# Kernel tuning notes

Hardware: AMD Instinct MI355X
Metric: run time of the kernel (lower is better)

## Reference

```python
import jax, jax.numpy as jnp
import numpy as np

B, T, E, H = 2, 1024, 2048, 32
D = E // H
GROUP = (0.25, 0.25, 0.25, 0.25)
NEG = float(np.finfo(np.float32).min)


def quant_per_token(t, n_bits):
    # smoothquant-style: clamp(absmax, 1e-5) / qmax, per last-dim row
    qmax = 2 ** (n_bits - 1) - 1
    s = jnp.clip(jnp.abs(t).max(-1, keepdims=True), 1e-5, None) / qmax
    return jnp.round(t / s) * s


def w8a8_linear(x, W, b, quant_out=False):
    xq = quant_per_token(x, 8)           # per-token act quant
    Wq = quant_per_token(W, 8)           # per-output-channel weight quant (W: [out, in])
    y = xq @ Wq.T + b
    return quant_per_token(y, 8) if quant_out else y


def to_heads(x):
    # [B, T, E] -> [B*H, T, D]
    return x.reshape(B, T, H, D).transpose(0, 2, 1, 3).reshape(B * H, T, D)


def setup_inputs() -> dict:
    key = jax.random.key(0)
    ks = jax.random.split(key, 9)
    hidden_states = jax.random.normal(ks[0], (B, T, E), jnp.float32)
    causal = jnp.where(jnp.tril(jnp.ones((T, T), bool)), 0.0, NEG).astype(jnp.float32)
    attention_mask = jnp.broadcast_to(causal[None, None], (B, 1, T, T))
    w = 0.02
    return {
        'hidden_states': hidden_states,
        'attention_mask': attention_mask,
        'Wq': jax.random.normal(ks[1], (E, E), jnp.float32) * w,
        'bq': jax.random.normal(ks[2], (E,), jnp.float32) * w,
        'Wk': jax.random.normal(ks[3], (E, E), jnp.float32) * w,
        'bk': jax.random.normal(ks[4], (E,), jnp.float32) * w,
        'Wv': jax.random.normal(ks[5], (E, E), jnp.float32) * w,
        'bv': jax.random.normal(ks[6], (E,), jnp.float32) * w,
        'Wo': jax.random.normal(ks[7], (E, E), jnp.float32) * w,
        'bo': jax.random.normal(ks[8], (E,), jnp.float32) * w,
    }


def reference(hidden_states, attention_mask, Wq, bq, Wk, bk, Wv, bv, Wo, bo):
    scaling = D ** -0.5
    q = w8a8_linear(hidden_states, Wq, bq, quant_out=True) * scaling  # [B,T,E]
    k = w8a8_linear(hidden_states, Wk, bk)                            # [B,T,E]
    v = w8a8_linear(hidden_states, Wv, bv)                            # [B,T,E]

    # ---- heavy-hitter scoring pass (pre-4bit-quant K) ----
    q1, k1 = to_heads(q), to_heads(k)                                 # [BH,T,D]
    aw = jnp.einsum('btd,bsd->bts', q1, k1)                           # [BH,T,T]
    aw = aw.reshape(B, H, T, T) + attention_mask
    aw = jnp.maximum(aw, NEG).reshape(B * H, T, T)
    tmp_attn = jax.nn.softmax(aw, axis=-1)
    acc = tmp_attn.sum(axis=1).sum(axis=0)[None, :]                   # [1,T]
    row_vector = jnp.arange(T, 0, -1).astype(jnp.float32)[None, :]    # T, T-1, ..., 1
    acc = acc / row_vector / (B * H)

    # ---- group-wise top-k heavy-hitter selection ----
    range_size_or = int(T / len(GROUP) / 2)
    start = 1
    idx_list = []
    for i, ratio in enumerate(GROUP):
        rs = int(T * ratio)
        end = min(start + rs - 1, T) if i < len(GROUP) - 1 else T
        partial = acc[:, start - 1:end]
        _, ti = jax.lax.top_k(partial, range_size_or)
        idx_list.append(ti + start - 1)
        start = end + 1
    topk_idx = jnp.concatenate(idx_list, axis=-1).reshape(-1)

    # ---- mixed-precision K quantization ----
    k_abs = jnp.abs(k)
    # fake_quant_mix (8-bit): amax(...)[0] in torch indexes batch 0 -> scales [T,1]
    s_mix = jnp.clip(k_abs.max(-1, keepdims=True)[0] / 127.0, 1e-5, None)  # [T,1]
    k_imp = jnp.round(k / s_mix) * s_mix
    # fake_quant (4-bit, per-row): clamp then divide by 7
    s4 = jnp.clip(k_abs.max(-1, keepdims=True), 1e-5, None) / 7.0
    kq = jnp.round(k / s4) * s4
    kq = kq.at[:, topk_idx, :].set(k_imp[:, topk_idx, :])
    # fake_quant_v (4-bit, per-tensor)
    sv = jnp.clip(jnp.abs(v).max(), 1e-5, None) / 7.0
    vq = jnp.round(v / sv) * sv

    # ---- actual attention with quantized K/V ----
    q2, k2, v2 = to_heads(q), to_heads(kq), to_heads(vq)
    aw2 = jnp.einsum('btd,bsd->bts', q2, k2).reshape(B, H, T, T) + attention_mask
    aw2 = jnp.maximum(aw2, NEG).reshape(B * H, T, T)
    probs = jax.nn.softmax(aw2, axis=-1)
    out = jnp.einsum('bts,bsd->btd', probs, v2)                       # [BH,T,D]
    out = out.reshape(B, H, T, D).transpose(0, 2, 1, 3).reshape(B, T, E)
    return w8a8_linear(out, Wo, bo)
```

## Files before the change

### kernel.cpp

```cpp
#include <hip/hip_runtime.h>
#include <stdint.h>

#define NEG_INF (-__builtin_inff())
#define L2E 1.4426950408889634f

namespace {
constexpr int kT   = 1024;
constexpr int kE   = 2048;
}

using bf16x8 = __attribute__((ext_vector_type(8))) short;
using f32x4  = __attribute__((ext_vector_type(4))) float;
using i32x4  = __attribute__((ext_vector_type(4))) int;

#define MFMA_BF16(a, b, c) __builtin_amdgcn_mfma_f32_16x16x32_bf16((a), (b), (c), 0, 0, 0)
#define MFMA_I8(a, b, c)   __builtin_amdgcn_mfma_i32_16x16x64_i8((a), (b), (c), 0, 0, 0)

__device__ __forceinline__ void gload16(const void* g, void* l) {
  __builtin_amdgcn_global_load_lds((const __attribute__((address_space(1))) unsigned*)g,
                                   (__attribute__((address_space(3))) unsigned*)l, 16, 0, 0);
}
__device__ __forceinline__ unsigned bfr(float x) {
  unsigned u = __float_as_uint(x);
  return (u + 0x7FFFu + ((u >> 16) & 1u)) >> 16;
}
__device__ __forceinline__ float bf2f(unsigned h) { return __uint_as_float(h << 16); }
__device__ __forceinline__ unsigned pk2(float a, float b) { return bfr(a) | (bfr(b) << 16); }
__device__ __forceinline__ float fexp2(float x) { return __builtin_amdgcn_exp2f(x); }

__device__ __forceinline__ float waveReduceMax(float v) {
#pragma unroll
  for (int o = 32; o > 0; o >>= 1) v = fmaxf(v, __shfl_down(v, o, 64));
  return v;
}
__device__ __forceinline__ float waveReduceSum(float v) {
#pragma unroll
  for (int o = 32; o > 0; o >>= 1) v += __shfl_down(v, o, 64);
  return v;
}
__device__ __forceinline__ float blockMax256(float v, float* r4) {
  const int tid = threadIdx.x;
  float wm = waveReduceMax(v);
  if ((tid & 63) == 0) r4[tid >> 6] = wm;
  __syncthreads();
  float bm = fmaxf(fmaxf(r4[0], r4[1]), fmaxf(r4[2], r4[3]));
  __syncthreads();
  return bm;
}

__global__ __launch_bounds__(256) void k_rowquant_all(const float* __restrict__ Xh,
                                                      const float* __restrict__ W0,
                                                      const float* __restrict__ W1,
                                                      const float* __restrict__ W2,
                                                      const float* __restrict__ W3,
                                                      int8_t* __restrict__ Qh,
                                                      int8_t* __restrict__ Q0,
                                                      int8_t* __restrict__ Q1,
                                                      int8_t* __restrict__ Q2,
                                                      int8_t* __restrict__ Q3,
                                                      float* __restrict__ sX,
                                                      float* __restrict__ sWall,
                                                      unsigned* __restrict__ vmax) {
  const int y = blockIdx.y;
  const float* X = (y == 0) ? Xh : (y == 1) ? W0 : (y == 2) ? W1 : (y == 3) ? W2 : W3;
  int8_t* Qp = (y == 0) ? Qh : (y == 1) ? Q0 : (y == 2) ? Q1 : (y == 3) ? Q2 : Q3;
  const int row = blockIdx.x;
  const int tid = threadIdx.x;
  if (row == 0 && y == 0 && tid == 0) *vmax = 0u;
  const float* x = X + (size_t)row * kE;
  __shared__ float r4[4];
  float am = 0.f;
  float4 v[2];
#pragma unroll
  for (int it = 0; it < 2; ++it) {
    v[it] = *reinterpret_cast<const float4*>(x + (size_t)(it * 256 + tid) * 4);
    am = fmaxf(am, fmaxf(fmaxf(fabsf(v[it].x), fabsf(v[it].y)), fmaxf(fabsf(v[it].z), fabsf(v[it].w))));
  }
  const float bm = blockMax256(am, r4);
  const float s = fmaxf(bm, 1e-5f) / 127.f;
  int8_t* xq = Qp + (size_t)row * kE;
#pragma unroll
  for (int it = 0; it < 2; ++it) {
    const int i = (it * 256 + tid) * 4;
    char4 q;
    q.x = (char)(int)rintf(v[it].x / s);
    q.y = (char)(int)rintf(v[it].y / s);
    q.z = (char)(int)rintf(v[it].z / s);
    q.w = (char)(int)rintf(v[it].w / s);
    *reinterpret_cast<char4*>(xq + i) = q;
  }
  if (tid == 0) {
    if (y == 0) sX[row] = s;
    else sWall[(y - 1) * kE + row] = s;
  }
}

__global__ __launch_bounds__(256) void k_rowquant_i8(const float* __restrict__ X,
                                                     int8_t* __restrict__ Xq,
                                                     float* __restrict__ S) {
  const int row = blockIdx.x;
  const int tid = threadIdx.x;
  const float* x = X + (size_t)row * kE;
  __shared__ float r4[4];
  float am = 0.f;
  float4 v[2];
#pragma unroll
  for (int it = 0; it < 2; ++it) {
    v[it] = *reinterpret_cast<const float4*>(x + (size_t)(it * 256 + tid) * 4);
    am = fmaxf(am, fmaxf(fmaxf(fabsf(v[it].x), fabsf(v[it].y)), fmaxf(fabsf(v[it].z), fabsf(v[it].w))));
  }
  const float bm = blockMax256(am, r4);
  const float s = fmaxf(bm, 1e-5f) / 127.f;
  int8_t* xq = Xq + (size_t)row * kE;
#pragma unroll
  for (int it = 0; it < 2; ++it) {
    const int i = (it * 256 + tid) * 4;
    char4 q;
    q.x = (char)(int)rintf(v[it].x / s);
    q.y = (char)(int)rintf(v[it].y / s);
    q.z = (char)(int)rintf(v[it].z / s);
    q.w = (char)(int)rintf(v[it].w / s);
    *reinterpret_cast<char4*>(xq + i) = q;
  }
  if (tid == 0) S[row] = s;
}

__global__ __launch_bounds__(256) void k_prep(const float* __restrict__ Qb,
                                              const float* __restrict__ Kb,
                                              const float* __restrict__ Vb,
                                              short* __restrict__ qi,
                                              float* __restrict__ sqg,
                                              short* __restrict__ khi,
                                              short* __restrict__ klo,
                                              float* __restrict__ s4,
                                              float* __restrict__ smix,
                                              unsigned* __restrict__ vmax) {
  const int row = blockIdx.x;
  const int tid = threadIdx.x;
  __shared__ float r4[4];

  {
    const float* x = Qb + (size_t)row * kE;
    float am = 0.f;
    float4 v[2];
#pragma unroll
    for (int it = 0; it < 2; ++it) {
      v[it] = *reinterpret_cast<const float4*>(x + (size_t)(it * 256 + tid) * 4);
      am = fmaxf(am, fmaxf(fmaxf(fabsf(v[it].x), fabsf(v[it].y)), fmaxf(fabsf(v[it].z), fabsf(v[it].w))));
    }
    const float bm = blockMax256(am, r4);
    const float s = fmaxf(bm, 1e-5f) / 127.f;
#pragma unroll
    for (int it = 0; it < 2; ++it) {
      const int i = (it * 256 + tid) * 4;
      short4 q;
      q.x = (short)bfr(rintf(v[it].x / s));
      q.y = (short)bfr(rintf(v[it].y / s));
      q.z = (short)bfr(rintf(v[it].z / s));
      q.w = (short)bfr(rintf(v[it].w / s));
      *reinterpret_cast<short4*>(qi + (size_t)row * kE + i) = q;
    }
    if (tid == 0) sqg[row] = s * 0.125f;
  }

  {
    const float* x = Kb + (size_t)row * kE;
    float am = 0.f;
    float4 v[2];
#pragma unroll
    for (int it = 0; it < 2; ++it) {
      v[it] = *reinterpret_cast<const float4*>(x + (size_t)(it * 256 + tid) * 4);
      am = fmaxf(am, fmaxf(fmaxf(fabsf(v[it].x), fabsf(v[it].y)), fmaxf(fabsf(v[it].z), fabsf(v[it].w))));
    }
    const float bm = blockMax256(am, r4);
#pragma unroll
    for (int it = 0; it < 2; ++it) {
      const int i = (it * 256 + tid) * 4;
      short4 hh, ll;
      unsigned hb;
      hb = bfr(v[it].x); hh.x = (short)hb; ll.x = (short)bfr(v[it].x - bf2f(hb));
      hb = bfr(v[it].y); hh.y = (short)hb; ll.y = (short)bfr(v[it].y - bf2f(hb));
      hb = bfr(v[it].z); hh.z = (short)hb; ll.z = (short)bfr(v[it].z - bf2f(hb));
      hb = bfr(v[it].w); hh.w = (short)hb; ll.w = (short)bfr(v[it].w - bf2f(hb));
      *reinterpret_cast<short4*>(khi + (size_t)row * kE + i) = hh;
      *reinterpret_cast<short4*>(klo + (size_t)row * kE + i) = ll;
    }
    if (tid == 0) {
      s4[row] = fmaxf(bm, 1e-5f) / 7.f;
      if (row < kT) smix[row] = fmaxf(bm / 127.f, 1e-5f);
    }
  }

  {
    const float* x = Vb + (size_t)row * kE;
    float am = 0.f;
#pragma unroll
    for (int it = 0; it < 2; ++it) {
      const float4 v = *reinterpret_cast<const float4*>(x + (size_t)(it * 256 + tid) * 4);
      am = fmaxf(am, fmaxf(fmaxf(fabsf(v.x), fabsf(v.y)), fmaxf(fabsf(v.z), fabsf(v.w))));
    }
    const float bm = blockMax256(am, r4);
    if (tid == 0) atomicMax(vmax, __float_as_uint(bm));
  }
}

__global__ __launch_bounds__(256) void k_kint(const float* __restrict__ Kb,
                                              const float* __restrict__ s4,
                                              const float* __restrict__ smix,
                                              const int* __restrict__ sel,
                                              short* __restrict__ ki,
                                              float* __restrict__ skg) {
  const int row = blockIdx.x;
  const int tid = threadIdx.x;
  const int t = row & (kT - 1);
  const float s = sel[t] ? smix[t] : s4[row];
  const float* x = Kb + (size_t)row * kE;
#pragma unroll
  for (int it = 0; it < 2; ++it) {
    const int i = (it * 256 + tid) * 4;
    const float4 v = *reinterpret_cast<const float4*>(x + i);
    short4 q;
    q.x = (short)bfr(rintf(v.x / s));
    q.y = (short)bfr(rintf(v.y / s));
    q.z = (short)bfr(rintf(v.z / s));
    q.w = (short)bfr(rintf(v.w / s));
    *reinterpret_cast<short4*>(ki + (size_t)row * kE + i) = q;
  }
  if (tid == 0) skg[row] = s;
}

__global__ __launch_bounds__(256) void k_vint(const float* __restrict__ Vb,
                                              const unsigned* __restrict__ vmax,
                                              short* __restrict__ vt) {
  const int tt = blockIdx.x;
  const int bh = blockIdx.y;
  const int b = bh >> 5, h = bh & 31;
  const float sv = fmaxf(__uint_as_float(*vmax), 1e-5f) / 7.f;
  __shared__ short tr[64][80];
  const int tid = threadIdx.x;
#pragma unroll
  for (int i = 0; i < 4; ++i) {
    const int e = i * 256 + tid;
    const int tok = e >> 4, d4 = (e & 15) * 4;
    const float4 v = *reinterpret_cast<const float4*>(
        &Vb[(size_t)(b * kT + tt * 64 + tok) * kE + h * 64 + d4]);
    tr[d4 + 0][tok] = (short)bfr(rintf(v.x / sv));
    tr[d4 + 1][tok] = (short)bfr(rintf(v.y / sv));
    tr[d4 + 2][tok] = (short)bfr(rintf(v.z / sv));
    tr[d4 + 3][tok] = (short)bfr(rintf(v.w / sv));
  }
  __syncthreads();
#pragma unroll
  for (int i = 0; i < 2; ++i) {
    const int e = i * 256 + tid;
    const int d = e >> 3, u = e & 7;
    const bf16x8 row = *reinterpret_cast<const bf16x8*>(&tr[d][u * 8]);
    *reinterpret_cast<bf16x8*>(&vt[(size_t)(bh * 64 + d) * kT + tt * 64 + u * 8]) = row;
  }
}

__device__ __forceinline__ void gemm_i8_body(int m0, int n0,
                                             const int8_t* __restrict__ A,
                                             const float* __restrict__ sa,
                                             const int8_t* __restrict__ Bw,
                                             const float* __restrict__ sw,
                                             const float* __restrict__ bias,
                                             float* __restrict__ Y,
                                             int8_t* As0, int8_t* As1,
                                             int8_t* Bs0, int8_t* Bs1) {
  int8_t* Asb[2] = {As0, As1};
  int8_t* Bsb[2] = {Bs0, Bs1};
  const int tid = threadIdx.x;
  const int lane = tid & 63, w = tid >> 6;
  const int g = lane >> 4, c16 = lane & 15;
  const int wm = (w >> 1) * 64, wn = (w & 1) * 64;
  const int rsw = (c16 >> 1) & 3;

  const i32x4 zero = {0, 0, 0, 0};
  i32x4 acc[4][4];
#pragma unroll
  for (int i = 0; i < 4; ++i)
#pragma unroll
    for (int j = 0; j < 4; ++j) acc[i][j] = zero;

  const int srow = tid >> 2, su = tid & 3;
  const int ssw = (srow >> 1) & 3;
  auto stage = [&](int buf, int k0) {
#pragma unroll
    for (int i = 0; i < 2; ++i) {
      const int row = i * 64 + srow;
      const int uoff = ((su ^ ssw) << 4);
      gload16(A + (size_t)(m0 + row) * kE + k0 + uoff, &Asb[buf][row * 64 + su * 16]);
      gload16(Bw + (size_t)(n0 + row) * kE + k0 + uoff, &Bsb[buf][row * 64 + su * 16]);
    }
  };

  stage(0, 0);
  __syncthreads();
  int cur = 0;
  for (int k0 = 0; k0 < kE; k0 += 64) {
    if (k0 + 64 < kE) stage(cur ^ 1, k0 + 64);
    i32x4 av[4], bv[4];
#pragma unroll
    for (int f = 0; f < 4; ++f) {
      const int ar = wm + f * 16 + c16;
      av[f] = *reinterpret_cast<const i32x4*>(&Asb[cur][ar * 64 + ((g ^ rsw) << 4)]);
      const int br = wn + f * 16 + c16;
      bv[f] = *reinterpret_cast<const i32x4*>(&Bsb[cur][br * 64 + ((g ^ rsw) << 4)]);
    }
#pragma unroll
    for (int fm = 0; fm < 4; ++fm)
#pragma unroll
      for (int fn = 0; fn < 4; ++fn) acc[fm][fn] = MFMA_I8(av[fm], bv[fn], acc[fm][fn]);
    __syncthreads();
    cur ^= 1;
  }

#pragma unroll
  for (int fn = 0; fn < 4; ++fn) {
    const int n = n0 + wn + fn * 16 + c16;
    const float swn = sw[n], bn = bias[n];
#pragma unroll
    for (int fm = 0; fm < 4; ++fm) {
#pragma unroll
      for (int r = 0; r < 4; ++r) {
        const int m = m0 + wm + fm * 16 + g * 4 + r;
        Y[(size_t)m * kE + n] = (float)acc[fm][fn][r] * sa[m] * swn + bn;
      }
    }
  }
}

__global__ __launch_bounds__(256) void k_gemm_i8(const int8_t* __restrict__ A,
                                                 const float* __restrict__ sa,
                                                 const int8_t* __restrict__ Bw,
                                                 const float* __restrict__ sw,
                                                 const float* __restrict__ bias,
                                                 float* __restrict__ Y) {
  __shared__ int8_t As[2][128 * 64];
  __shared__ int8_t Bs[2][128 * 64];
  const int linear = blockIdx.x + (blockIdx.y << 4);
  const int nid = (linear & 7) * 32 + (linear >> 3);
  const int x = nid & 15, y = nid >> 4;
  gemm_i8_body(y * 128, x * 128, A, sa, Bw, sw, bias, Y, As[0], As[1], Bs[0], Bs[1]);
}

__global__ __launch_bounds__(256) void k_gemm_qkv(const int8_t* __restrict__ A,
                                                  const float* __restrict__ sa,
                                                  const int8_t* __restrict__ Wq,
                                                  const int8_t* __restrict__ Wk,
                                                  const int8_t* __restrict__ Wv,
                                                  const float* __restrict__ sWall,
                                                  const float* __restrict__ bq,
                                                  const float* __restrict__ bk,
                                                  const float* __restrict__ bv,
                                                  float* __restrict__ qb,
                                                  float* __restrict__ kb,
                                                  float* __restrict__ vb) {
  __shared__ int8_t As[2][128 * 64];
  __shared__ int8_t Bs[2][128 * 64];
  const int linear = blockIdx.x + (blockIdx.y << 4) + (blockIdx.z << 8);
  const int nid = (linear & 7) * 96 + (linear >> 3);
  const int x = nid & 15, y = (nid >> 4) & 15, z = nid >> 8;
  const int8_t* Bw = (z == 0) ? Wq : (z == 1) ? Wk : Wv;
  const float* sw = sWall + (size_t)z * kE;
  const float* bias = (z == 0) ? bq : (z == 1) ? bk : bv;
  float* Y = (z == 0) ? qb : (z == 1) ? kb : vb;
  gemm_i8_body(y * 128, x * 128, A, sa, Bw, sw, bias, Y, As[0], As[1], Bs[0], Bs[1]);
}

__global__ __launch_bounds__(256) void k_attn1(const short* __restrict__ qi,
                                               const short* __restrict__ khi,
                                               const short* __restrict__ klo,
                                               const float* __restrict__ sqg,
                                               float* __restrict__ accPart) {
  const int r1 = blockIdx.x, r2 = 15 - r1, bh = blockIdx.y;
  const int b = bh >> 5, h = bh & 31;
  const int tid = threadIdx.x, lane = tid & 63, w = tid >> 6;
  const int g = lane >> 4, c16 = lane & 15;
  const int swz = c16 & 7;

  __shared__ short qs1[64 * 64];
  __shared__ short qs2[64 * 64];
  __shared__ short hbuf[2][64 * 64];
  __shared__ short lbuf[2][64 * 64];
  __shared__ float accL[1024];
  __shared__ float Arow[128], Crow[128];

  for (int i = tid; i < 1024; i += 256) accL[i] = 0.f;

  const int st8 = tid >> 3, su = tid & 7;
  {
    const int tokb1 = b * kT + r1 * 64;
    const int tokb2 = b * kT + r2 * 64;
#pragma unroll
    for (int i = 0; i < 2; ++i) {
      const int tok = i * 32 + st8;
      const int co = ((su ^ (tok & 7)) << 3);
      gload16(qi + (size_t)(tokb1 + tok) * kE + h * 64 + co, &qs1[tok * 64 + su * 8]);
      gload16(qi + (size_t)(tokb2 + tok) * kE + h * 64 + co, &qs2[tok * 64 + su * 8]);
    }
  }
  auto stage = [&](int buf, int kt) {
    const int tokb = b * kT + kt * 64;
#pragma unroll
    for (int i = 0; i < 2; ++i) {
      const int tok = i * 32 + st8;
      const size_t gsrc = (size_t)(tokb + tok) * kE + h * 64 + ((su ^ (tok & 7)) << 3);
      gload16(khi + gsrc, &hbuf[buf][tok * 64 + su * 8]);
      gload16(klo + gsrc, &lbuf[buf][tok * 64 + su * 8]);
    }
  };

  stage(0, 0);
  __syncthreads();

  const int qrow = w * 16 + c16;
  const bf16x8 q1_0 = *reinterpret_cast<const bf16x8*>(&qs1[qrow * 64 + ((g ^ swz) << 3)]);
  const bf16x8 q1_1 = *reinterpret_cast<const bf16x8*>(&qs1[qrow * 64 + (((4 + g) ^ swz) << 3)]);
  const bf16x8 q2_0 = *reinterpret_cast<const bf16x8*>(&qs2[qrow * 64 + ((g ^ swz) << 3)]);
  const bf16x8 q2_1 = *reinterpret_cast<const bf16x8*>(&qs2[qrow * 64 + (((4 + g) ^ swz) << 3)]);
  const float A1c = sqg[b * kT + r1 * 64 + qrow] * L2E;
  const float A2c = sqg[b * kT + r2 * 64 + qrow] * L2E;

  float m1 = NEG_INF, l1 = 0.f, m2_ = NEG_INF, l2 = 0.f;
  int cur = 0;

  for (int kt = 0; kt <= r2; ++kt) {
    if (kt < r2) stage(cur ^ 1, kt + 1);
    const bool act1 = kt <= r1;
    float p1[4][4], p2[4][4];
    float pm1 = NEG_INF, pm2 = NEG_INF;
#pragma unroll
    for (int f = 0; f < 4; ++f) {
      const int tokl = f * 16 + c16;
      const bf16x8 ah0 = *reinterpret_cast<const bf16x8*>(&hbuf[cur][tokl * 64 + ((g ^ swz) << 3)]);
      const bf16x8 ah1 = *reinterpret_cast<const bf16x8*>(&hbuf[cur][tokl * 64 + (((4 + g) ^ swz) << 3)]);
      const bf16x8 al0 = *reinterpret_cast<const bf16x8*>(&lbuf[cur][tokl * 64 + ((g ^ swz) << 3)]);
      const bf16x8 al1 = *reinterpret_cast<const bf16x8*>(&lbuf[cur][tokl * 64 + (((4 + g) ^ swz) << 3)]);
      f32x4 sB = {0.f, 0.f, 0.f, 0.f};
      sB = MFMA_BF16(ah0, q2_0, sB);
      sB = MFMA_BF16(ah1, q2_1, sB);
      sB = MFMA_BF16(al0, q2_0, sB);
      sB = MFMA_BF16(al1, q2_1, sB);
      f32x4 sA = {0.f, 0.f, 0.f, 0.f};
      if (act1) {
        sA = MFMA_BF16(ah0, q1_0, sA);
        sA = MFMA_BF16(ah1, q1_1, sA);
        sA = MFMA_BF16(al0, q1_0, sA);
        sA = MFMA_BF16(al1, q1_1, sA);
      }
#pragma unroll
      for (int r = 0; r < 4; ++r) {
        const int tokd = f * 16 + g * 4 + r;
        float s2 = sB[r] * A2c;
        if (kt == r2 && tokd > qrow) s2 = NEG_INF;
        p2[f][r] = s2;
        pm2 = fmaxf(pm2, s2);
        float s1 = sA[r] * A1c;
        if (kt == r1 && tokd > qrow) s1 = NEG_INF;
        p1[f][r] = s1;
        pm1 = fmaxf(pm1, s1);
      }
    }
    {
      pm2 = fmaxf(pm2, __shfl_xor(pm2, 16));
      pm2 = fmaxf(pm2, __shfl_xor(pm2, 32));
      const bool upd = pm2 > m2_ + 8.f;
      const float mn = upd ? fmaxf(m2_, pm2) : m2_;
      const float fsc = fexp2(m2_ - mn);
      float rs = 0.f;
#pragma unroll
      for (int f = 0; f < 4; ++f)
#pragma unroll
        for (int r = 0; r < 4; ++r) rs += fexp2(p2[f][r] - mn);
      rs += __shfl_xor(rs, 16);
      rs += __shfl_xor(rs, 32);
      l2 = l2 * fsc + rs;
      m2_ = mn;
    }
    if (act1) {
      pm1 = fmaxf(pm1, __shfl_xor(pm1, 16));
      pm1 = fmaxf(pm1, __shfl_xor(pm1, 32));
      const bool upd = pm1 > m1 + 8.f;
      const float mn = upd ? fmaxf(m1, pm1) : m1;
      const float fsc = fexp2(m1 - mn);
      float rs = 0.f;
#pragma unroll
      for (int f = 0; f < 4; ++f)
#pragma unroll
        for (int r = 0; r < 4; ++r) rs += fexp2(p1[f][r] - mn);
      rs += __shfl_xor(rs, 16);
      rs += __shfl_xor(rs, 32);
      l1 = l1 * fsc + rs;
      m1 = mn;
    }
    __syncthreads();
    cur ^= 1;
  }

  if (g == 0) {
    Arow[qrow] = A1c;
    Crow[qrow] = -(m1 + __builtin_amdgcn_logf(l1));
    Arow[64 + qrow] = A2c;
    Crow[64 + qrow] = -(m2_ + __builtin_amdgcn_logf(l2));
  }
  stage(0, 0);
  __syncthreads();

  bf16x8 qa1_0[4], qa1_1[4], qa2_0[4], qa2_1[4];
  float Ar1[4][4], Cr1[4][4], Ar2[4][4], Cr2[4][4];
#pragma unroll
  for (int f = 0; f < 4; ++f) {
    const int qr = f * 16 + c16;
    qa1_0[f] = *reinterpret_cast<const bf16x8*>(&qs1[qr * 64 + ((g ^ swz) << 3)]);
    qa1_1[f] = *reinterpret_cast<const bf16x8*>(&qs1[qr * 64 + (((4 + g) ^ swz) << 3)]);
    qa2_0[f] = *reinterpret_cast<const bf16x8*>(&qs2[qr * 64 + ((g ^ swz) << 3)]);
    qa2_1[f] = *reinterpret_cast<const bf16x8*>(&qs2[qr * 64 + (((4 + g) ^ swz) << 3)]);
#pragma unroll
    for (int r = 0; r < 4; ++r) {
      const int tokd = f * 16 + g * 4 + r;
      Ar1[f][r] = Arow[tokd];
      Cr1[f][r] = Crow[tokd];
      Ar2[f][r] = Arow[64 + tokd];
      Cr2[f][r] = Crow[64 + tokd];
    }
  }

  const int ktokL = w * 16 + c16;
  cur = 0;
  for (int kt = 0; kt <= r2; ++kt) {
    if (kt < r2) stage(cur ^ 1, kt + 1);
    const bf16x8 kh0 = *reinterpret_cast<const bf16x8*>(&hbuf[cur][ktokL * 64 + ((g ^ swz) << 3)]);
    const bf16x8 kh1 = *reinterpret_cast<const bf16x8*>(&hbuf[cur][ktokL * 64 + (((4 + g) ^ swz) << 3)]);
    const bf16x8 kl0 = *reinterpret_cast<const bf16x8*>(&lbuf[cur][ktokL * 64 + ((g ^ swz) << 3)]);
    const bf16x8 kl1 = *reinterpret_cast<const bf16x8*>(&lbuf[cur][ktokL * 64 + (((4 + g) ^ swz) << 3)]);
    float csum = 0.f;
    if (kt < r2) {
#pragma unroll
      for (int f = 0; f < 4; ++f) {
        f32x4 sf = {0.f, 0.f, 0.f, 0.f};
        sf = MFMA_BF16(qa2_0[f], kh0, sf);
        sf = MFMA_BF16(qa2_1[f], kh1, sf);
        sf = MFMA_BF16(qa2_0[f], kl0, sf);
        sf = MFMA_BF16(qa2_1[f], kl1, sf);
#pragma unroll
        for (int r = 0; r < 4; ++r) csum += fexp2(fmaf(sf[r], Ar2[f][r], Cr2[f][r]));
      }
    } else {
#pragma unroll
      for (int f = 0; f < 4; ++f) {
        f32x4 sf = {0.f, 0.f, 0.f, 0.f};
        sf = MFMA_BF16(qa2_0[f], kh0, sf);
        sf = MFMA_BF16(qa2_1[f], kh1, sf);
        sf = MFMA_BF16(qa2_0[f], kl0, sf);
        sf = MFMA_BF16(qa2_1[f], kl1, sf);
#pragma unroll
        for (int r = 0; r < 4; ++r) {
          const float v = fexp2(fmaf(sf[r], Ar2[f][r], Cr2[f][r]));
          if (ktokL <= (f * 16 + g * 4 + r)) csum += v;
        }
      }
    }
    if (kt <= r1) {
      if (kt < r1) {
#pragma unroll
        for (int f = 0; f < 4; ++f) {
          f32x4 sf = {0.f, 0.f, 0.f, 0.f};
          sf = MFMA_BF16(qa1_0[f], kh0, sf);
          sf = MFMA_BF16(qa1_1[f], kh1, sf);
          sf = MFMA_BF16(qa1_0[f], kl0, sf);
          sf = MFMA_BF16(qa1_1[f], kl1, sf);
#pragma unroll
          for (int r = 0; r < 4; ++r) csum += fexp2(fmaf(sf[r], Ar1[f][r], Cr1[f][r]));
        }
      } else {
#pragma unroll
        for (int f = 0; f < 4; ++f) {
          f32x4 sf = {0.f, 0.f, 0.f, 0.f};
          sf = MFMA_BF16(qa1_0[f], kh0, sf);
          sf = MFMA_BF16(qa1_1[f], kh1, sf);
          sf = MFMA_BF16(qa1_0[f], kl0, sf);
          sf = MFMA_BF16(qa1_1[f], kl1, sf);
#pragma unroll
          for (int r = 0; r < 4; ++r) {
            const float v = fexp2(fmaf(sf[r], Ar1[f][r], Cr1[f][r]));
            if (ktokL <= (f * 16 + g * 4 + r)) csum += v;
          }
        }
      }
    }
    csum += __shfl_xor(csum, 16);
    csum += __shfl_xor(csum, 32);
    if (g == 0) accL[kt * 64 + ktokL] += csum;
    __syncthreads();
    cur ^= 1;
  }

  for (int i = tid; i < 1024; i += 256)
    accPart[(size_t)(bh * 8 + r1) * 1024 + i] = accL[i];
}

__global__ __launch_bounds__(256) void k_accreduce(const float* __restrict__ part,
                                                   float* __restrict__ acc) {
  const int j = blockIdx.x;
  const int tid = threadIdx.x;
  float s = 0.f;
  for (int p = tid; p < 512; p += 256) s += part[(size_t)p * 1024 + j];
  __shared__ float r4[4];
  const float ws = waveReduceSum(s);
  if ((tid & 63) == 0) r4[tid >> 6] = ws;
  __syncthreads();
  if (tid == 0) {
    const float t = r4[0] + r4[1] + r4[2] + r4[3];
    acc[j] = t / (float)(kT - j) / 64.f;
  }
}

__global__ __launch_bounds__(256) void k_topk(const float* __restrict__ acc,
                                              int* __restrict__ sel) {
  const int gq = blockIdx.x;
  const int i = threadIdx.x;
  __shared__ float v[256];
  const float vi = acc[gq * 256 + i];
  v[i] = vi;
  __syncthreads();
  int rank = 0;
  for (int j = 0; j < 256; ++j) {
    const float vj = v[j];
    rank += (vj > vi) || (vj == vi && j < i);
  }
  sel[gq * 256 + i] = (rank < 128) ? 1 : 0;
}

__global__ __launch_bounds__(256) void k_attn2(const short* __restrict__ qi,
                                               const short* __restrict__ ki,
                                               const short* __restrict__ vt,
                                               const float* __restrict__ sqg,
                                               const float* __restrict__ skg,
                                               const unsigned* __restrict__ vmax,
                                               float* __restrict__ ctx) {
  const int r1 = blockIdx.x, r2 = 15 - r1, bh = blockIdx.y;
  const int b = bh >> 5, h = bh & 31;
  const int tid = threadIdx.x, lane = tid & 63, w = tid >> 6;
  const int g = lane >> 4, c16 = lane & 15;
  const int swz = c16 & 7;
  const int wrow = w * 16 + c16;

  __shared__ short kbuf[2][64 * 64];
  __shared__ short vbuf[2][64 * 64];
  __shared__ float skl[2][64];

  const int qtokA = b * kT + r1 * 64 + wrow;
  const int qtokB = b * kT + r2 * 64 + wrow;
  bf16x8 qfA[2], qfB[2];
  qfA[0] = *reinterpret_cast<const bf16x8*>(qi + (size_t)qtokA * kE + h * 64 + g * 8);
  qfA[1] = *reinterpret_cast<const bf16x8*>(qi + (size_t)qtokA * kE + h * 64 + 32 + g * 8);
  qfB[0] = *reinterpret_cast<const bf16x8*>(qi + (size_t)qtokB * kE + h * 64 + g * 8);
  qfB[1] = *reinterpret_cast<const bf16x8*>(qi + (size_t)qtokB * kE + h * 64 + 32 + g * 8);
  const float sqA = sqg[qtokA] * L2E;
  const float sqB = sqg[qtokB] * L2E;
  const float sv = fmaxf(__uint_as_float(*vmax), 1e-5f) / 7.f;

  const int st8 = tid >> 3, su = tid & 7;
  auto stage = [&](int buf, int kt) {
    const int tokb = b * kT + kt * 64;
#pragma unroll
    for (int i = 0; i < 2; ++i) {
      const int tok = i * 32 + st8;
      gload16(ki + (size_t)(tokb + tok) * kE + h * 64 + ((su ^ (tok & 7)) << 3),
              &kbuf[buf][tok * 64 + su * 8]);
      gload16(vt + (size_t)(bh * 64 + tok) * kT + kt * 64 + ((su ^ (tok & 7)) << 3),
              &vbuf[buf][tok * 64 + su * 8]);
    }
    if (tid < 64) skl[buf][tid] = skg[tokb + tid];
  };

  float mA = NEG_INF, lA = 0.f, mB = NEG_INF, lB = 0.f;
  f32x4 otA[4], otB[4];
#pragma unroll
  for (int f = 0; f < 4; ++f) {
    otA[f] = (f32x4){0.f, 0.f, 0.f, 0.f};
    otB[f] = (f32x4){0.f, 0.f, 0.f, 0.f};
  }

  stage(0, 0);
  __syncthreads();
  int cur = 0;

  const int srcLo = c16 | ((g & 1) << 5);
  const int srcHi = srcLo | 16;
  const bool selq = ((g >> 1) & 1) != 0;

  for (int kt = 0; kt <= r2; ++kt) {
    if (kt < r2) stage(cur ^ 1, kt + 1);
    const bool act1 = kt <= r1;

    f32x4 sfB4[4], sfA4[4];
#pragma unroll
    for (int f = 0; f < 4; ++f) {
      const int tokl = f * 16 + c16;
      const bf16x8 k0 = *reinterpret_cast<const bf16x8*>(&kbuf[cur][tokl * 64 + ((g ^ swz) << 3)]);
      const bf16x8 k1 = *reinterpret_cast<const bf16x8*>(&kbuf[cur][tokl * 64 + (((4 + g) ^ swz) << 3)]);
      f32x4 s = {0.f, 0.f, 0.f, 0.f};
      s = MFMA_BF16(k0, qfB[0], s);
      s = MFMA_BF16(k1, qfB[1], s);
      sfB4[f] = s;
      f32x4 sa = {0.f, 0.f, 0.f, 0.f};
      if (act1) {
        sa = MFMA_BF16(k0, qfA[0], sa);
        sa = MFMA_BF16(k1, qfA[1], sa);
      }
      sfA4[f] = sa;
    }

    {
      float p[4][4];
      float pm = NEG_INF;
#pragma unroll
      for (int f = 0; f < 4; ++f)
#pragma unroll
        for (int r = 0; r < 4; ++r) {
          const int tokd = f * 16 + g * 4 + r;
          float s2 = sfB4[f][r] * skl[cur][tokd] * sqB;
          if (kt == r2 && tokd > wrow) s2 = NEG_INF;
          p[f][r] = s2;
          pm = fmaxf(pm, s2);
        }
      pm = fmaxf(pm, __shfl_xor(pm, 16));
      pm = fmaxf(pm, __shfl_xor(pm, 32));
      const bool upd = pm > mB + 8.f;
      const float mn = upd ? fmaxf(mB, pm) : mB;
      const float fsc = fexp2(mB - mn);
      mB = mn;
      float rs = 0.f;
#pragma unroll
      for (int f = 0; f < 4; ++f)
#pragma unroll
        for (int r = 0; r < 4; ++r) {
          const float e = fexp2(p[f][r] - mn);
          p[f][r] = e;
          rs += e;
        }
      rs += __shfl_xor(rs, 16);
      rs += __shfl_xor(rs, 32);
      lB = lB * fsc + rs;
      if (__any(upd)) {
#pragma unroll
        for (int f = 0; f < 4; ++f)
#pragma unroll
          for (int r = 0; r < 4; ++r) otB[f][r] *= fsc;
      }
#pragma unroll
      for (int c = 0; c < 2; ++c) {
        const unsigned q0a = pk2(p[2 * c][0], p[2 * c][1]);
        const unsigned q0b = pk2(p[2 * c][2], p[2 * c][3]);
        const unsigned q1a = pk2(p[2 * c + 1][0], p[2 * c + 1][1]);
        const unsigned q1b = pk2(p[2 * c + 1][2], p[2 * c + 1][3]);
        unsigned a0, a1;
        union { unsigned u[4]; bf16x8 v; } Bh;
        a0 = __shfl(q0a, srcLo); a1 = __shfl(q1a, srcLo); Bh.u[0] = selq ? a1 : a0;
        a0 = __shfl(q0b, srcLo); a1 = __shfl(q1b, srcLo); Bh.u[1] = selq ? a1 : a0;
        a0 = __shfl(q0a, srcHi); a1 = __shfl(q1a, srcHi); Bh.u[2] = selq ? a1 : a0;
        a0 = __shfl(q0b, srcHi); a1 = __shfl(q1b, srcHi); Bh.u[3] = selq ? a1 : a0;
#pragma unroll
        for (int fd = 0; fd < 4; ++fd) {
          const int d = fd * 16 + c16;
          const bf16x8 va = *reinterpret_cast<const bf16x8*>(
              &vbuf[cur][d * 64 + ((((c << 2) | g) ^ swz) << 3)]);
          otB[fd] = MFMA_BF16(va, Bh.v, otB[fd]);
        }
      }
    }

    if (act1) {
      float p[4][4];
      float pm = NEG_INF;
#pragma unroll
      for (int f = 0; f < 4; ++f)
#pragma unroll
        for (int r = 0; r < 4; ++r) {
          const int tokd = f * 16 + g * 4 + r;
          float s2 = sfA4[f][r] * skl[cur][tokd] * sqA;
          if (kt == r1 && tokd > wrow) s2 = NEG_INF;
          p[f][r] = s2;
          pm = fmaxf(pm, s2);
        }
      pm = fmaxf(pm, __shfl_xor(pm, 16));
      pm = fmaxf(pm, __shfl_xor(pm, 32));
      const bool upd = pm > mA + 8.f;
      const float mn = upd ? fmaxf(mA, pm) : mA;
      const float fsc = fexp2(mA - mn);
      mA = mn;
      float rs = 0.f;
#pragma unroll
      for (int f = 0; f < 4; ++f)
#pragma unroll
        for (int r = 0; r < 4; ++r) {
          const float e = fexp2(p[f][r] - mn);
          p[f][r] = e;
          rs += e;
        }
      rs += __shfl_xor(rs, 16);
      rs += __shfl_xor(rs, 32);
      lA = lA * fsc + rs;
      if (__any(upd)) {
#pragma unroll
        for (int f = 0; f < 4; ++f)
#pragma unroll
          for (int r = 0; r < 4; ++r) otA[f][r] *= fsc;
      }
#pragma unroll
      for (int c = 0; c < 2; ++c) {
        const unsigned q0a = pk2(p[2 * c][0], p[2 * c][1]);
        const unsigned q0b = pk2(p[2 * c][2], p[2 * c][3]);
        const unsigned q1a = pk2(p[2 * c + 1][0], p[2 * c + 1][1]);
        const unsigned q1b = pk2(p[2 * c + 1][2], p[2 * c + 1][3]);
        unsigned a0, a1;
        union { unsigned u[4]; bf16x8 v; } Bh;
        a0 = __shfl(q0a, srcLo); a1 = __shfl(q1a, srcLo); Bh.u[0] = selq ? a1 : a0;
        a0 = __shfl(q0b, srcLo); a1 = __shfl(q1b, srcLo); Bh.u[1] = selq ? a1 : a0;
        a0 = __shfl(q0a, srcHi); a1 = __shfl(q1a, srcHi); Bh.u[2] = selq ? a1 : a0;
        a0 = __shfl(q0b, srcHi); a1 = __shfl(q1b, srcHi); Bh.u[3] = selq ? a1 : a0;
#pragma unroll
        for (int fd = 0; fd < 4; ++fd) {
          const int d = fd * 16 + c16;
          const bf16x8 va = *reinterpret_cast<const bf16x8*>(
              &vbuf[cur][d * 64 + ((((c << 2) | g) ^ swz) << 3)]);
          otA[fd] = MFMA_BF16(va, Bh.v, otA[fd]);
        }
      }
    }

    __syncthreads();
    cur ^= 1;
  }

  const float ilA = sv / lA;
  const float ilB = sv / lB;
#pragma unroll
  for (int fd = 0; fd < 4; ++fd) {
    float4 oA, oB;
    oA.x = otA[fd][0] * ilA; oA.y = otA[fd][1] * ilA;
    oA.z = otA[fd][2] * ilA; oA.w = otA[fd][3] * ilA;
    oB.x = otB[fd][0] * ilB; oB.y = otB[fd][1] * ilB;
    oB.z = otB[fd][2] * ilB; oB.w = otB[fd][3] * ilB;
    *reinterpret_cast<float4*>(&ctx[(size_t)qtokA * kE + h * 64 + fd * 16 + g * 4]) = oA;
    *reinterpret_cast<float4*>(&ctx[(size_t)qtokB * kE + h * 64 + fd * 16 + g * 4]) = oB;
  }
}

extern "C" void kernel_launch(void* const* d_in, const int* in_sizes, int n_in,
                              void* d_out, int out_size, void* d_ws, size_t ws_size,
                              hipStream_t stream) {
  (void)in_sizes; (void)n_in; (void)out_size; (void)ws_size;
  const float* hs = (const float*)d_in[0];
  const float* Wq = (const float*)d_in[2];
  const float* bq = (const float*)d_in[3];
  const float* Wk = (const float*)d_in[4];
  const float* bk = (const float*)d_in[5];
  const float* Wv = (const float*)d_in[6];
  const float* bv = (const float*)d_in[7];
  const float* Wo = (const float*)d_in[8];
  const float* bo = (const float*)d_in[9];
  float* out = (float*)d_out;

  char* p = (char*)d_ws;
  auto take = [&](size_t bytes) {
    char* r = p;
    p += (bytes + 255) & ~(size_t)255;
    return r;
  };
  float* qb  = (float*)take((size_t)2048 * 2048 * 4);
  float* kb  = (float*)take((size_t)2048 * 2048 * 4);
  float* vb  = (float*)take((size_t)2048 * 2048 * 4);
  float* ctx = (float*)take((size_t)2048 * 2048 * 4);
  short* qiB = (short*)take((size_t)2048 * 2048 * 2);
  int8_t* xq  = (int8_t*)take((size_t)2048 * 2048);
  int8_t* woq = (int8_t*)take((size_t)2048 * 2048);
  float* sX    = (float*)take(2048 * 4);
  float* sWall = (float*)take(4 * 2048 * 4);
  float* sC    = (float*)take(2048 * 4);
  float* s4v   = (float*)take(2048 * 4);
  float* smix  = (float*)take(1024 * 4);
  float* accv  = (float*)take(1024 * 4);
  int*   sel   = (int*)take(1024 * 4);
  float* sqg   = (float*)take(2048 * 4);
  float* skg   = (float*)take(2048 * 4);
  unsigned* vmax = (unsigned*)take(256);

  short* khi = (short*)qb;
  short* klo = (short*)qb + (size_t)2048 * 2048;
  short* kint = khi;
  short* vtp  = klo;
  float* accPart = ctx;
  int8_t* wqq = (int8_t*)ctx + ((size_t)2 << 20);
  int8_t* wkq = (int8_t*)ctx + ((size_t)6 << 20);
  int8_t* wvq = (int8_t*)ctx + ((size_t)10 << 20);
  int8_t* cq = xq;

  k_rowquant_all<<<dim3(2048, 5), 256, 0, stream>>>(hs, Wq, Wk, Wv, Wo,
                                                    xq, wqq, wkq, wvq, woq,
                                                    sX, sWall, vmax);

  k_gemm_qkv<<<dim3(16, 16, 3), 256, 0, stream>>>(xq, sX, wqq, wkq, wvq, sWall,
                                                  bq, bk, bv, qb, kb, vb);

  k_prep<<<2048, 256, 0, stream>>>(qb, kb, vb, qiB, sqg, khi, klo, s4v, smix, vmax);

  k_attn1<<<dim3(8, 64), 256, 0, stream>>>(qiB, khi, klo, sqg, accPart);
  k_accreduce<<<1024, 256, 0, stream>>>(accPart, accv);
  k_topk<<<4, 256, 0, stream>>>(accv, sel);

  k_kint<<<2048, 256, 0, stream>>>(kb, s4v, smix, sel, kint, skg);
  k_vint<<<dim3(16, 64), 256, 0, stream>>>(vb, vmax, vtp);

  k_attn2<<<dim3(8, 64), 256, 0, stream>>>(qiB, kint, vtp, sqg, skg, vmax, ctx);

  k_rowquant_i8<<<2048, 256, 0, stream>>>(ctx, cq, sC);
  k_gemm_i8<<<dim3(16, 16), 256, 0, stream>>>(cq, sC, woq, sWall + 3 * 2048, bo, out);
}
```

Before: 232.6 us.

## Retile int8 GEMMs to 32x32 MFMA, fuse K/V quant and top-k kernels

The int8 GEMMs move from 16x16x64 MFMA with 128x128 tiles and 256 threads to 32x32x32 MFMA with 256x128 tiles and 512 threads. This aims to raise operand reuse per LDS read and cut the number of blocks. The K and V quantization kernels are merged into one launch, and the partial-sum reduction is merged with top-k selection. Attention MFMA sections get s_setprio hints. The merged reduction now runs a 512-step serial loop in each of only 1024 threads, which could be latency-bound.

```diff
diff --git a/kernel.cpp b/kernel.cpp
--- a/kernel.cpp
+++ b/kernel.cpp
@@ -12,9 +12,10 @@
 using bf16x8 = __attribute__((ext_vector_type(8))) short;
 using f32x4  = __attribute__((ext_vector_type(4))) float;
 using i32x4  = __attribute__((ext_vector_type(4))) int;
+using i32x16 = __attribute__((ext_vector_type(16))) int;
 
 #define MFMA_BF16(a, b, c) __builtin_amdgcn_mfma_f32_16x16x32_bf16((a), (b), (c), 0, 0, 0)
-#define MFMA_I8(a, b, c)   __builtin_amdgcn_mfma_i32_16x16x64_i8((a), (b), (c), 0, 0, 0)
+#define MFMA_I8_32(a, b, c) __builtin_amdgcn_mfma_i32_32x32x32_i8((a), (b), (c), 0, 0, 0)
 
 __device__ __forceinline__ void gload16(const void* g, void* l) {
   __builtin_amdgcn_global_load_lds((const __attribute__((address_space(1))) unsigned*)g,
@@ -31,11 +32,6 @@
 __device__ __forceinline__ float waveReduceMax(float v) {
 #pragma unroll
   for (int o = 32; o > 0; o >>= 1) v = fmaxf(v, __shfl_down(v, o, 64));
-  return v;
-}
-__device__ __forceinline__ float waveReduceSum(float v) {
-#pragma unroll
-  for (int o = 32; o > 0; o >>= 1) v += __shfl_down(v, o, 64);
   return v;
 }
 __device__ __forceinline__ float blockMax256(float v, float* r4) {
@@ -204,58 +200,59 @@
   }
 }
 
-__global__ __launch_bounds__(256) void k_kint(const float* __restrict__ Kb,
-                                              const float* __restrict__ s4,
-                                              const float* __restrict__ smix,
-                                              const int* __restrict__ sel,
-                                              short* __restrict__ ki,
-                                              float* __restrict__ skg) {
-  const int row = blockIdx.x;
+__global__ __launch_bounds__(256) void k_kvint(const float* __restrict__ Kb,
+                                               const float* __restrict__ s4,
+                                               const float* __restrict__ smix,
+                                               const int* __restrict__ sel,
+                                               short* __restrict__ ki,
+                                               float* __restrict__ skg,
+                                               const float* __restrict__ Vb,
+                                               const unsigned* __restrict__ vmax,
+                                               short* __restrict__ vt) {
+  const int bid = blockIdx.x;
   const int tid = threadIdx.x;
-  const int t = row & (kT - 1);
-  const float s = sel[t] ? smix[t] : s4[row];
-  const float* x = Kb + (size_t)row * kE;
-#pragma unroll
-  for (int it = 0; it < 2; ++it) {
-    const int i = (it * 256 + tid) * 4;
-    const float4 v = *reinterpret_cast<const float4*>(x + i);
-    short4 q;
-    q.x = (short)bfr(rintf(v.x / s));
-    q.y = (short)bfr(rintf(v.y / s));
-    q.z = (short)bfr(rintf(v.z / s));
-    q.w = (short)bfr(rintf(v.w / s));
-    *reinterpret_cast<short4*>(ki + (size_t)row * kE + i) = q;
-  }
-  if (tid == 0) skg[row] = s;
-}
-
-__global__ __launch_bounds__(256) void k_vint(const float* __restrict__ Vb,
-                                              const unsigned* __restrict__ vmax,
-                                              short* __restrict__ vt) {
-  const int tt = blockIdx.x;
-  const int bh = blockIdx.y;
-  const int b = bh >> 5, h = bh & 31;
-  const float sv = fmaxf(__uint_as_float(*vmax), 1e-5f) / 7.f;
-  __shared__ short tr[64][80];
-  const int tid = threadIdx.x;
-#pragma unroll
-  for (int i = 0; i < 4; ++i) {
-    const int e = i * 256 + tid;
-    const int tok = e >> 4, d4 = (e & 15) * 4;
-    const float4 v = *reinterpret_cast<const float4*>(
-        &Vb[(size_t)(b * kT + tt * 64 + tok) * kE + h * 64 + d4]);
-    tr[d4 + 0][tok] = (short)bfr(rintf(v.x / sv));
-    tr[d4 + 1][tok] = (short)bfr(rintf(v.y / sv));
-    tr[d4 + 2][tok] = (short)bfr(rintf(v.z / sv));
-    tr[d4 + 3][tok] = (short)bfr(rintf(v.w / sv));
-  }
-  __syncthreads();
-#pragma unroll
-  for (int i = 0; i < 2; ++i) {
-    const int e = i * 256 + tid;
-    const int d = e >> 3, u = e & 7;
-    const bf16x8 row = *reinterpret_cast<const bf16x8*>(&tr[d][u * 8]);
-    *reinterpret_cast<bf16x8*>(&vt[(size_t)(bh * 64 + d) * kT + tt * 64 + u * 8]) = row;
+  if (bid < 2048) {
+    const int row = bid;
+    const int t = row & (kT - 1);
+    const float s = sel[t] ? smix[t] : s4[row];
+    const float* x = Kb + (size_t)row * kE;
+#pragma unroll
+    for (int it = 0; it < 2; ++it) {
+      const int i = (it * 256 + tid) * 4;
+      const float4 v = *reinterpret_cast<const float4*>(x + i);
+      short4 q;
+      q.x = (short)bfr(rintf(v.x / s));
+      q.y = (short)bfr(rintf(v.y / s));
+      q.z = (short)bfr(rintf(v.z / s));
+      q.w = (short)bfr(rintf(v.w / s));
+      *reinterpret_cast<short4*>(ki + (size_t)row * kE + i) = q;
+    }
+    if (tid == 0) skg[row] = s;
+  } else {
+    const int t = bid - 2048;
+    const int tt = t & 15, bh = t >> 4;
+    const int b = bh >> 5, h = bh & 31;
+    const float sv = fmaxf(__uint_as_float(*vmax), 1e-5f) / 7.f;
+    __shared__ short tr[64][80];
+#pragma unroll
+    for (int i = 0; i < 4; ++i) {
+      const int e = i * 256 + tid;
+      const int tok = e >> 4, d4 = (e & 15) * 4;
+      const float4 v = *reinterpret_cast<const float4*>(
+          &Vb[(size_t)(b * kT + tt * 64 + tok) * kE + h * 64 + d4]);
+      tr[d4 + 0][tok] = (short)bfr(rintf(v.x / sv));
+      tr[d4 + 1][tok] = (short)bfr(rintf(v.y / sv));
+      tr[d4 + 2][tok] = (short)bfr(rintf(v.z / sv));
+      tr[d4 + 3][tok] = (short)bfr(rintf(v.w / sv));
+    }
+    __syncthreads();
+#pragma unroll
+    for (int i = 0; i < 2; ++i) {
+      const int e = i * 256 + tid;
+      const int d = e >> 3, u = e & 7;
+      const bf16x8 row = *reinterpret_cast<const bf16x8*>(&tr[d][u * 8]);
+      *reinterpret_cast<bf16x8*>(&vt[(size_t)(bh * 64 + d) * kT + tt * 64 + u * 8]) = row;
+    }
   }
 }
 
@@ -266,86 +263,94 @@
                                              const float* __restrict__ sw,
                                              const float* __restrict__ bias,
                                              float* __restrict__ Y,
-                                             int8_t* As0, int8_t* As1,
-                                             int8_t* Bs0, int8_t* Bs1) {
-  int8_t* Asb[2] = {As0, As1};
-  int8_t* Bsb[2] = {Bs0, Bs1};
+                                             int8_t* AsBase, int8_t* BsBase) {
   const int tid = threadIdx.x;
   const int lane = tid & 63, w = tid >> 6;
-  const int g = lane >> 4, c16 = lane & 15;
-  const int wm = (w >> 1) * 64, wn = (w & 1) * 64;
-  const int rsw = (c16 >> 1) & 3;
-
-  const i32x4 zero = {0, 0, 0, 0};
-  i32x4 acc[4][4];
-#pragma unroll
-  for (int i = 0; i < 4; ++i)
-#pragma unroll
-    for (int j = 0; j < 4; ++j) acc[i][j] = zero;
-
-  const int srow = tid >> 2, su = tid & 3;
-  const int ssw = (srow >> 1) & 3;
+  const int l31 = lane & 31, lh = lane >> 5;
+  const int wmRow = (w >> 1) * 64, wnRow = (w & 1) * 64;
+
+  const i32x16 zero16 = {0};
+  i32x16 acc00 = zero16, acc01 = zero16, acc10 = zero16, acc11 = zero16;
+
   auto stage = [&](int buf, int k0) {
+    int8_t* As = AsBase + buf * 16384;
+    int8_t* Bs = BsBase + buf * 8192;
 #pragma unroll
     for (int i = 0; i < 2; ++i) {
-      const int row = i * 64 + srow;
-      const int uoff = ((su ^ ssw) << 4);
-      gload16(A + (size_t)(m0 + row) * kE + k0 + uoff, &Asb[buf][row * 64 + su * 16]);
-      gload16(Bw + (size_t)(n0 + row) * kE + k0 + uoff, &Bsb[buf][row * 64 + su * 16]);
+      const int s = tid + i * 512;
+      const int row = s >> 2, gp = s & 3;
+      const int gs = gp ^ ((row >> 1) & 3);
+      gload16(A + (size_t)(m0 + row) * kE + k0 + gs * 16, As + s * 16);
+    }
+    {
+      const int row = tid >> 2, gp = tid & 3;
+      const int gs = gp ^ ((row >> 1) & 3);
+      gload16(Bw + (size_t)(n0 + row) * kE + k0 + gs * 16, Bs + tid * 16);
     }
   };
 
   stage(0, 0);
   __syncthreads();
   int cur = 0;
+
+  const int ar0 = wmRow + l31, ar1 = wmRow + 32 + l31;
+  const int br0 = wnRow + l31, br1 = wnRow + 32 + l31;
+  const int sa0 = (ar0 >> 1) & 3, sa1 = (ar1 >> 1) & 3;
+  const int sb0 = (br0 >> 1) & 3, sb1 = (br1 >> 1) & 3;
+
   for (int k0 = 0; k0 < kE; k0 += 64) {
     if (k0 + 64 < kE) stage(cur ^ 1, k0 + 64);
-    i32x4 av[4], bv[4];
-#pragma unroll
-    for (int f = 0; f < 4; ++f) {
-      const int ar = wm + f * 16 + c16;
-      av[f] = *reinterpret_cast<const i32x4*>(&Asb[cur][ar * 64 + ((g ^ rsw) << 4)]);
-      const int br = wn + f * 16 + c16;
-      bv[f] = *reinterpret_cast<const i32x4*>(&Bsb[cur][br * 64 + ((g ^ rsw) << 4)]);
-    }
-#pragma unroll
-    for (int fm = 0; fm < 4; ++fm)
-#pragma unroll
-      for (int fn = 0; fn < 4; ++fn) acc[fm][fn] = MFMA_I8(av[fm], bv[fn], acc[fm][fn]);
+    const int8_t* As = AsBase + cur * 16384;
+    const int8_t* Bs = BsBase + cur * 8192;
+#pragma unroll
+    for (int j = 0; j < 2; ++j) {
+      const int gn = lh + 2 * j;
+      const i32x4 a0 = *reinterpret_cast<const i32x4*>(As + ((ar0 << 2) + (gn ^ sa0)) * 16);
+      const i32x4 a1 = *reinterpret_cast<const i32x4*>(As + ((ar1 << 2) + (gn ^ sa1)) * 16);
+      const i32x4 b0 = *reinterpret_cast<const i32x4*>(Bs + ((br0 << 2) + (gn ^ sb0)) * 16);
+      const i32x4 b1 = *reinterpret_cast<const i32x4*>(Bs + ((br1 << 2) + (gn ^ sb1)) * 16);
+      acc00 = MFMA_I8_32(a0, b0, acc00);
+      acc01 = MFMA_I8_32(a0, b1, acc01);
+      acc10 = MFMA_I8_32(a1, b0, acc10);
+      acc11 = MFMA_I8_32(a1, b1, acc11);
+    }
     __syncthreads();
     cur ^= 1;
   }
 
 #pragma unroll
-  for (int fn = 0; fn < 4; ++fn) {
-    const int n = n0 + wn + fn * 16 + c16;
-    const float swn = sw[n], bn = bias[n];
-#pragma unroll
-    for (int fm = 0; fm < 4; ++fm) {
-#pragma unroll
-      for (int r = 0; r < 4; ++r) {
-        const int m = m0 + wm + fm * 16 + g * 4 + r;
-        Y[(size_t)m * kE + n] = (float)acc[fm][fn][r] * sa[m] * swn + bn;
-      }
-    }
-  }
-}
-
-__global__ __launch_bounds__(256) void k_gemm_i8(const int8_t* __restrict__ A,
+  for (int fn = 0; fn < 2; ++fn) {
+    const int col = n0 + wnRow + fn * 32 + l31;
+    const float swn = sw[col], bn = bias[col];
+#pragma unroll
+    for (int fm = 0; fm < 2; ++fm) {
+      const i32x16 accv = (fm == 0) ? ((fn == 0) ? acc00 : acc01)
+                                    : ((fn == 0) ? acc10 : acc11);
+      const int r0 = m0 + wmRow + fm * 32 + 4 * lh;
+#pragma unroll
+      for (int reg = 0; reg < 16; ++reg) {
+        const int row = r0 + (reg & 3) + 8 * (reg >> 2);
+        Y[(size_t)row * kE + col] = (float)accv[reg] * sa[row] * swn + bn;
+      }
+    }
+  }
+}
+
+__global__ __launch_bounds__(512) void k_gemm_i8(const int8_t* __restrict__ A,
                                                  const float* __restrict__ sa,
                                                  const int8_t* __restrict__ Bw,
                                                  const float* __restrict__ sw,
                                                  const float* __restrict__ bias,
                                                  float* __restrict__ Y) {
-  __shared__ int8_t As[2][128 * 64];
-  __shared__ int8_t Bs[2][128 * 64];
+  __shared__ int8_t As[2 * 16384];
+  __shared__ int8_t Bs[2 * 8192];
   const int linear = blockIdx.x + (blockIdx.y << 4);
-  const int nid = (linear & 7) * 32 + (linear >> 3);
+  const int nid = (linear & 7) * 16 + (linear >> 3);
   const int x = nid & 15, y = nid >> 4;
-  gemm_i8_body(y * 128, x * 128, A, sa, Bw, sw, bias, Y, As[0], As[1], Bs[0], Bs[1]);
-}
-
-__global__ __launch_bounds__(256) void k_gemm_qkv(const int8_t* __restrict__ A,
+  gemm_i8_body(y * 256, x * 128, A, sa, Bw, sw, bias, Y, As, Bs);
+}
+
+__global__ __launch_bounds__(512) void k_gemm_qkv(const int8_t* __restrict__ A,
                                                   const float* __restrict__ sa,
                                                   const int8_t* __restrict__ Wq,
                                                   const int8_t* __restrict__ Wk,
@@ -357,16 +362,16 @@
                                                   float* __restrict__ qb,
                                                   float* __restrict__ kb,
                                                   float* __restrict__ vb) {
-  __shared__ int8_t As[2][128 * 64];
-  __shared__ int8_t Bs[2][128 * 64];
-  const int linear = blockIdx.x + (blockIdx.y << 4) + (blockIdx.z << 8);
-  const int nid = (linear & 7) * 96 + (linear >> 3);
-  const int x = nid & 15, y = (nid >> 4) & 15, z = nid >> 8;
+  __shared__ int8_t As[2 * 16384];
+  __shared__ int8_t Bs[2 * 8192];
+  const int linear = blockIdx.x + (blockIdx.y << 4) + (blockIdx.z << 7);
+  const int nid = (linear & 7) * 48 + (linear >> 3);
+  const int x = nid & 15, y = (nid >> 4) & 7, z = nid >> 7;
   const int8_t* Bw = (z == 0) ? Wq : (z == 1) ? Wk : Wv;
   const float* sw = sWall + (size_t)z * kE;
   const float* bias = (z == 0) ? bq : (z == 1) ? bk : bv;
   float* Y = (z == 0) ? qb : (z == 1) ? kb : vb;
-  gemm_i8_body(y * 128, x * 128, A, sa, Bw, sw, bias, Y, As[0], As[1], Bs[0], Bs[1]);
+  gemm_i8_body(y * 256, x * 128, A, sa, Bw, sw, bias, Y, As, Bs);
 }
 
 __global__ __launch_bounds__(256) void k_attn1(const short* __restrict__ qi,
@@ -431,6 +436,7 @@
     const bool act1 = kt <= r1;
     float p1[4][4], p2[4][4];
     float pm1 = NEG_INF, pm2 = NEG_INF;
+    __builtin_amdgcn_s_setprio(1);
 #pragma unroll
     for (int f = 0; f < 4; ++f) {
       const int tokl = f * 16 + c16;
@@ -463,6 +469,7 @@
         pm1 = fmaxf(pm1, s1);
       }
     }
+    __builtin_amdgcn_s_setprio(0);
     {
       pm2 = fmaxf(pm2, __shfl_xor(pm2, 16));
       pm2 = fmaxf(pm2, __shfl_xor(pm2, 32));
@@ -536,6 +543,7 @@
     const bf16x8 kl0 = *reinterpret_cast<const bf16x8*>(&lbuf[cur][ktokL * 64 + ((g ^ swz) << 3)]);
     const bf16x8 kl1 = *reinterpret_cast<const bf16x8*>(&lbuf[cur][ktokL * 64 + (((4 + g) ^ swz) << 3)]);
     float csum = 0.f;
+    __builtin_amdgcn_s_setprio(1);
     if (kt < r2) {
 #pragma unroll
       for (int f = 0; f < 4; ++f) {
@@ -590,6 +598,7 @@
         }
       }
     }
+    __builtin_amdgcn_s_setprio(0);
     csum += __shfl_xor(csum, 16);
     csum += __shfl_xor(csum, 32);
     if (g == 0) accL[kt * 64 + ktokL] += csum;
@@ -601,36 +610,22 @@
     accPart[(size_t)(bh * 8 + r1) * 1024 + i] = accL[i];
 }
 
-__global__ __launch_bounds__(256) void k_accreduce(const float* __restrict__ part,
-                                                   float* __restrict__ acc) {
-  const int j = blockIdx.x;
-  const int tid = threadIdx.x;
+__global__ __launch_bounds__(256) void k_acctopk(const float* __restrict__ part,
+                                                 int* __restrict__ sel) {
+  const int i = threadIdx.x;
+  const int j = blockIdx.x * 256 + i;
   float s = 0.f;
-  for (int p = tid; p < 512; p += 256) s += part[(size_t)p * 1024 + j];
-  __shared__ float r4[4];
-  const float ws = waveReduceSum(s);
-  if ((tid & 63) == 0) r4[tid >> 6] = ws;
-  __syncthreads();
-  if (tid == 0) {
-    const float t = r4[0] + r4[1] + r4[2] + r4[3];
-    acc[j] = t / (float)(kT - j) / 64.f;
-  }
-}
-
-__global__ __launch_bounds__(256) void k_topk(const float* __restrict__ acc,
-                                              int* __restrict__ sel) {
-  const int gq = blockIdx.x;
-  const int i = threadIdx.x;
+  for (int p = 0; p < 512; ++p) s += part[(size_t)p * 1024 + j];
+  const float vi = s / (float)(kT - j) / 64.f;
   __shared__ float v[256];
-  const float vi = acc[gq * 256 + i];
   v[i] = vi;
   __syncthreads();
   int rank = 0;
-  for (int j = 0; j < 256; ++j) {
-    const float vj = v[j];
-    rank += (vj > vi) || (vj == vi && j < i);
-  }
-  sel[gq * 256 + i] = (rank < 128) ? 1 : 0;
+  for (int jj = 0; jj < 256; ++jj) {
+    const float vj = v[jj];
+    rank += (vj > vi) || (vj == vi && jj < i);
+  }
+  sel[j] = (rank < 128) ? 1 : 0;
 }
 
 __global__ __launch_bounds__(256) void k_attn2(const short* __restrict__ qi,
@@ -697,6 +692,7 @@
     const bool act1 = kt <= r1;
 
     f32x4 sfB4[4], sfA4[4];
+    __builtin_amdgcn_s_setprio(1);
 #pragma unroll
     for (int f = 0; f < 4; ++f) {
       const int tokl = f * 16 + c16;
@@ -713,6 +709,7 @@
       }
       sfA4[f] = sa;
     }
+    __builtin_amdgcn_s_setprio(0);
 
     {
       float p[4][4];
@@ -763,6 +760,7 @@
         a0 = __shfl(q0b, srcLo); a1 = __shfl(q1b, srcLo); Bh.u[1] = selq ? a1 : a0;
         a0 = __shfl(q0a, srcHi); a1 = __shfl(q1a, srcHi); Bh.u[2] = selq ? a1 : a0;
         a0 = __shfl(q0b, srcHi); a1 = __shfl(q1b, srcHi); Bh.u[3] = selq ? a1 : a0;
+        __builtin_amdgcn_s_setprio(1);
 #pragma unroll
         for (int fd = 0; fd < 4; ++fd) {
           const int d = fd * 16 + c16;
@@ -770,6 +768,7 @@
               &vbuf[cur][d * 64 + ((((c << 2) | g) ^ swz) << 3)]);
           otB[fd] = MFMA_BF16(va, Bh.v, otB[fd]);
         }
+        __builtin_amdgcn_s_setprio(0);
       }
     }
 
@@ -822,6 +821,7 @@
         a0 = __shfl(q0b, srcLo); a1 = __shfl(q1b, srcLo); Bh.u[1] = selq ? a1 : a0;
         a0 = __shfl(q0a, srcHi); a1 = __shfl(q1a, srcHi); Bh.u[2] = selq ? a1 : a0;
         a0 = __shfl(q0b, srcHi); a1 = __shfl(q1b, srcHi); Bh.u[3] = selq ? a1 : a0;
+        __builtin_amdgcn_s_setprio(1);
 #pragma unroll
         for (int fd = 0; fd < 4; ++fd) {
           const int d = fd * 16 + c16;
@@ -829,6 +829,7 @@
               &vbuf[cur][d * 64 + ((((c << 2) | g) ^ swz) << 3)]);
           otA[fd] = MFMA_BF16(va, Bh.v, otA[fd]);
         }
+        __builtin_amdgcn_s_setprio(0);
       }
     }
 
@@ -883,7 +884,6 @@
   float* sC    = (float*)take(2048 * 4);
   float* s4v   = (float*)take(2048 * 4);
   float* smix  = (float*)take(1024 * 4);
-  float* accv  = (float*)take(1024 * 4);
   int*   sel   = (int*)take(1024 * 4);
   float* sqg   = (float*)take(2048 * 4);
   float* skg   = (float*)take(2048 * 4);
@@ -903,20 +903,18 @@
                                                     xq, wqq, wkq, wvq, woq,
                                                     sX, sWall, vmax);
 
-  k_gemm_qkv<<<dim3(16, 16, 3), 256, 0, stream>>>(xq, sX, wqq, wkq, wvq, sWall,
-                                                  bq, bk, bv, qb, kb, vb);
+  k_gemm_qkv<<<dim3(16, 8, 3), 512, 0, stream>>>(xq, sX, wqq, wkq, wvq, sWall,
+                                                 bq, bk, bv, qb, kb, vb);
 
   k_prep<<<2048, 256, 0, stream>>>(qb, kb, vb, qiB, sqg, khi, klo, s4v, smix, vmax);
 
   k_attn1<<<dim3(8, 64), 256, 0, stream>>>(qiB, khi, klo, sqg, accPart);
-  k_accreduce<<<1024, 256, 0, stream>>>(accPart, accv);
-  k_topk<<<4, 256, 0, stream>>>(accv, sel);
-
-  k_kint<<<2048, 256, 0, stream>>>(kb, s4v, smix, sel, kint, skg);
-  k_vint<<<dim3(16, 64), 256, 0, stream>>>(vb, vmax, vtp);
+  k_acctopk<<<4, 256, 0, stream>>>(accPart, sel);
+
+  k_kvint<<<3072, 256, 0, stream>>>(kb, s4v, smix, sel, kint, skg, vb, vmax, vtp);
 
   k_attn2<<<dim3(8, 64), 256, 0, stream>>>(qiB, kint, vtp, sqg, skg, vmax, ctx);
 
   k_rowquant_i8<<<2048, 256, 0, stream>>>(ctx, cq, sC);
-  k_gemm_i8<<<dim3(16, 16), 256, 0, stream>>>(cq, sC, woq, sWall + 3 * 2048, bo, out);
-}
+  k_gemm_i8<<<dim3(16, 8), 512, 0, stream>>>(cq, sC, woq, sWall + 3 * 2048, bo, out);
+}
```

Result: slower. 239.6 us (+3.0%).
